# Kernel optimization log

Measured on AMD Instinct MI355X. Metric: run time of the kernel, lower is better.

The kernel has to match this reference:

```python
import jax, jax.numpy as jnp
import numpy as np
from jax import lax

B, L, C = 8, 2048, 512
H = 8
D = C // H  # head_dim = 64
FF = 4 * C


def layer_norm(x, g, b, eps=1e-5):
    mu = jnp.mean(x, axis=-1, keepdims=True)
    var = jnp.mean((x - mu) ** 2, axis=-1, keepdims=True)
    return (x - mu) * lax.rsqrt(var + eps) * g + b


def conv1d(x, w, b, groups=1):
    # x: [N, Cin, L], w: [Cout, Cin//groups, K], 'same' padding for K=3
    y = lax.conv_general_dilated(
        x, w, window_strides=(1,), padding=[(1, 1)],
        dimension_numbers=('NCH', 'OIH', 'NCH'), feature_group_count=groups)
    return y + b[None, :, None]


def setup_inputs() -> dict:
    key = jax.random.key(0)
    ks = jax.random.split(key, 12)
    s = 0.02
    inp = {
        'x': jax.random.normal(ks[0], (B, L, C), dtype=jnp.float32),
        # norm1
        'g1': jnp.ones((C,), jnp.float32), 'b1': jnp.zeros((C,), jnp.float32),
        # attention projections (stored as [in, out] for x @ W)
        'qk_w': jax.random.normal(ks[1], (C, 2 * C), jnp.float32) * s,
        'qk_b': jnp.zeros((2 * C,), jnp.float32),
        'v_w': jax.random.normal(ks[2], (C, C), jnp.float32) * s,
        'v_b': jnp.zeros((C,), jnp.float32),
        # depthwise LePE conv: [D, 1, 3], groups=D
        'lepe_w': jax.random.normal(ks[3], (D, 1, 3), jnp.float32) * s,
        'lepe_b': jnp.zeros((D,), jnp.float32),
        # norm2
        'g2': jnp.ones((C,), jnp.float32), 'b2': jnp.zeros((C,), jnp.float32),
        # GatedConv1D: inner LayerNorm + Conv1d(C, 2C, 3, pad=1); proj_out=Identity (expansion=1)
        'spn_g': jnp.ones((C,), jnp.float32), 'spn_b': jnp.zeros((C,), jnp.float32),
        'sp_cw': jax.random.normal(ks[4], (2 * C, C, 3), jnp.float32) * s,
        'sp_cb': jnp.zeros((2 * C,), jnp.float32),
        # norm3
        'g3': jnp.ones((C,), jnp.float32), 'b3': jnp.zeros((C,), jnp.float32),
        # FFN
        'w1': jax.random.normal(ks[5], (C, FF), jnp.float32) * s,
        'bb1': jnp.zeros((FF,), jnp.float32),
        'w2': jax.random.normal(ks[6], (FF, C), jnp.float32) * s,
        'bb2': jnp.zeros((C,), jnp.float32),
    }
    return inp


def _attn(x, qk_w, qk_b, v_w, v_b, lepe_w, lepe_b):
    # x: [B, L, C]
    qk = (x @ qk_w + qk_b).reshape(B, L, 2, H, D).transpose(2, 0, 3, 1, 4)
    q, k = qk[0], qk[1]                      # [B, H, L, D]
    v = (x @ v_w + v_b).reshape(B, L, H, D).transpose(0, 2, 1, 3)  # [B, H, L, D]
    q = jax.nn.elu(q) + 1.0
    k = jax.nn.elu(k) + 1.0

    def lepe(t):
        # Faithful to torch: raw row-major reshape [B,H,L,D] -> [B*H, D, L]
        # (NOT a transpose), depthwise conv along last axis, reshape back.
        c = conv1d(t.reshape(B * H, D, L), lepe_w, lepe_b, groups=D)
        return t + c.reshape(B, H, D, L).transpose(0, 1, 3, 2)

    q = lepe(q)
    k = lepe(k)
    k_mean = jnp.mean(k, axis=2, keepdims=True)                    # [B, H, 1, D]
    z = 1.0 / (jnp.einsum('bhld,bhmd->bhlm', q, k_mean) + 1e-6)    # [B, H, L, 1]
    kv = jnp.einsum('bhld,bhle->bhde', k, v) / L                   # [B, H, D, D]
    out = jnp.einsum('bhld,bhde->bhle', q, kv) * z                 # [B, H, L, D]
    return out.transpose(0, 2, 1, 3).reshape(B, L, C)


def reference(x, g1, b1, qk_w, qk_b, v_w, v_b, lepe_w, lepe_b,
              g2, b2, spn_g, spn_b, sp_cw, sp_cb, g3, b3, w1, bb1, w2, bb2):
    # Dropout is identity (eval mode).
    # Block 1: linear attention with LePE
    x = x + _attn(layer_norm(x, g1, b1), qk_w, qk_b, v_w, v_b, lepe_w, lepe_b)

    # Block 2: gated conv state path. state_path(input) = input + gated(conv(LN(input)))
    sp_in = layer_norm(x, g2, b2)
    h = layer_norm(sp_in, spn_g, spn_b)
    c = conv1d(h.transpose(0, 2, 1), sp_cw, sp_cb).transpose(0, 2, 1)  # [B, L, 2C]
    vv, gg = jnp.split(c, 2, axis=-1)
    x = x + (sp_in + vv * jax.nn.sigmoid(gg))

    # Block 3: FFN with exact GELU (torch default)
    h = layer_norm(x, g3, b3)
    x = x + (jax.nn.gelu(h @ w1 + bb1, approximate=False) @ w2 + bb2)
    return x
```

## Files before the change

### kernel.cpp

```cpp
#include <hip/hip_runtime.h>
#include <hip/hip_bf16.h>
#include <math.h>

#define Bb 8
#define Ll 2048
#define Ccn 512
#define Hh 8
#define Dd 64
#define NR (Bb * Ll)
#define PROW 2050

typedef __hip_bfloat16 bf16;
typedef __attribute__((ext_vector_type(8))) __bf16 bf16x8;
typedef __attribute__((ext_vector_type(4))) float f32x4;

#define GLDS(g, l) __builtin_amdgcn_global_load_lds(                          \
    (const __attribute__((address_space(1))) void*)(g),                       \
    (__attribute__((address_space(3))) void*)(l), 16, 0, 0)

__device__ __forceinline__ void unpack2(unsigned u, float& a, float& b) {
  union { float f; unsigned x; } lo, hi;
  lo.x = u << 16; hi.x = u & 0xffff0000u;
  a = lo.f; b = hi.f;
}

__device__ __forceinline__ float frcp(float x) { return __builtin_amdgcn_rcpf(x); }

__device__ __forceinline__ float ldin(const void* p, int i, int isbf) {
  return isbf ? (float)((const bf16*)p)[i] : ((const float*)p)[i];
}

__device__ __forceinline__ void ldin8(const void* p, size_t base, int isbf, float* v) {
  if (isbf) {
    int4 q = *(const int4*)((const bf16*)p + base);
    unpack2((unsigned)q.x, v[0], v[1]); unpack2((unsigned)q.y, v[2], v[3]);
    unpack2((unsigned)q.z, v[4], v[5]); unpack2((unsigned)q.w, v[6], v[7]);
  } else {
    float4 a = *(const float4*)((const float*)p + base);
    float4 b = *(const float4*)((const float*)p + base + 4);
    v[0]=a.x; v[1]=a.y; v[2]=a.z; v[3]=a.w;
    v[4]=b.x; v[5]=b.y; v[6]=b.z; v[7]=b.w;
  }
}

__device__ __forceinline__ void st8(bf16* dst, const float* v) {
  bf16x8 o;
#pragma unroll
  for (int t = 0; t < 8; ++t) o[t] = (__bf16)v[t];
  *(bf16x8*)dst = o;
}

__global__ void detect_kernel(const unsigned* __restrict__ g1, int* __restrict__ flag) {
  *flag = ((g1[0] & 0xFFFFu) == 0x3F80u) ? 1 : 0;
}

__global__ void ln1_kernel(const void* __restrict__ x, const void* __restrict__ g,
                           const void* __restrict__ b, const int* __restrict__ dflag,
                           bf16* __restrict__ outb, float* __restrict__ xf)
{
  int isbf = *dflag;
  int row  = blockIdx.x * 4 + (threadIdx.x >> 6);
  int lane = threadIdx.x & 63;
  size_t obase = (size_t)row * Ccn + lane * 8;
  float vals[8];
  ldin8(x, obase, isbf, vals);
  float4 c0 = {vals[0], vals[1], vals[2], vals[3]};
  float4 c1 = {vals[4], vals[5], vals[6], vals[7]};
  *(float4*)(xf + obase)     = c0;
  *(float4*)(xf + obase + 4) = c1;
  float s = 0.f, q = 0.f;
#pragma unroll
  for (int a = 0; a < 8; ++a) { s += vals[a]; q += vals[a] * vals[a]; }
#pragma unroll
  for (int off = 1; off < 64; off <<= 1) {
    s += __shfl_xor(s, off);
    q += __shfl_xor(q, off);
  }
  float mu  = s * (1.f / Ccn);
  float var = q * (1.f / Ccn) - mu * mu;
  float rs  = rsqrtf(var + 1e-5f);
  float gv[8], bv[8], o[8];
  ldin8(g, lane * 8, isbf, gv);
  ldin8(b, lane * 8, isbf, bv);
#pragma unroll
  for (int a = 0; a < 8; ++a) o[a] = (vals[a] - mu) * rs * gv[a] + bv[a];
  st8(&outb[obase], o);
}

__global__ void ln_kernel(const float* __restrict__ xin, const void* __restrict__ g,
                          const void* __restrict__ b, const int* __restrict__ dflag,
                          bf16* __restrict__ outb)
{
  int isbf = *dflag;
  int row  = blockIdx.x * 4 + (threadIdx.x >> 6);
  int lane = threadIdx.x & 63;
  const float* xr = xin + (size_t)row * Ccn;
  float4 v0 = *(const float4*)(xr + lane * 8);
  float4 v1 = *(const float4*)(xr + lane * 8 + 4);
  float vals[8] = {v0.x, v0.y, v0.z, v0.w, v1.x, v1.y, v1.z, v1.w};
  float s = 0.f, q = 0.f;
#pragma unroll
  for (int a = 0; a < 8; ++a) { s += vals[a]; q += vals[a] * vals[a]; }
#pragma unroll
  for (int off = 1; off < 64; off <<= 1) {
    s += __shfl_xor(s, off);
    q += __shfl_xor(q, off);
  }
  float mu  = s * (1.f / Ccn);
  float var = q * (1.f / Ccn) - mu * mu;
  float rs  = rsqrtf(var + 1e-5f);
  size_t obase = (size_t)row * Ccn + lane * 8;
  float gv[8], bv[8], o[8];
  ldin8(g, lane * 8, isbf, gv);
  ldin8(b, lane * 8, isbf, bv);
#pragma unroll
  for (int a = 0; a < 8; ++a) o[a] = (vals[a] - mu) * rs * gv[a] + bv[a];
  st8(&outb[obase], o);
}

__global__ void glng_kernel(float* __restrict__ xf, const bf16* __restrict__ spin,
                            const bf16* __restrict__ c, const void* __restrict__ g,
                            const void* __restrict__ b, const int* __restrict__ dflag,
                            bf16* __restrict__ outb)
{
  int isbf = *dflag;
  int row  = blockIdx.x * 4 + (threadIdx.x >> 6);
  int lane = threadIdx.x & 63;
  size_t obase = (size_t)row * Ccn + lane * 8;
  int cc = lane * 8;
  float vv[8], gg[8], sp[8], xv[8];
  ldin8(&c[(size_t)row * 1024 + cc], 0, 1, vv);
  ldin8(&c[(size_t)row * 1024 + 512 + cc], 0, 1, gg);
  ldin8(&spin[obase], 0, 1, sp);
  float4 a0 = *(const float4*)&xf[obase];
  float4 a1 = *(const float4*)&xf[obase + 4];
  xv[0]=a0.x; xv[1]=a0.y; xv[2]=a0.z; xv[3]=a0.w;
  xv[4]=a1.x; xv[5]=a1.y; xv[6]=a1.z; xv[7]=a1.w;
#pragma unroll
  for (int a = 0; a < 8; ++a) xv[a] += sp[a] + vv[a] * frcp(1.f + __expf(-gg[a]));
  float4 o0 = {xv[0], xv[1], xv[2], xv[3]};
  float4 o1 = {xv[4], xv[5], xv[6], xv[7]};
  *(float4*)&xf[obase]     = o0;
  *(float4*)&xf[obase + 4] = o1;
  float s = 0.f, q = 0.f;
#pragma unroll
  for (int a = 0; a < 8; ++a) { s += xv[a]; q += xv[a] * xv[a]; }
#pragma unroll
  for (int off = 1; off < 64; off <<= 1) {
    s += __shfl_xor(s, off);
    q += __shfl_xor(q, off);
  }
  float mu  = s * (1.f / Ccn);
  float var = q * (1.f / Ccn) - mu * mu;
  float rs  = rsqrtf(var + 1e-5f);
  float gv[8], bv[8], o[8];
  ldin8(g, lane * 8, isbf, gv);
  ldin8(b, lane * 8, isbf, bv);
#pragma unroll
  for (int a = 0; a < 8; ++a) o[a] = (xv[a] - mu) * rs * gv[a] + bv[a];
  st8(&outb[obase], o);
}

__global__ void ln2_kernel(const float* __restrict__ xin, const void* __restrict__ g,
                           const void* __restrict__ b, const void* __restrict__ sg,
                           const void* __restrict__ sb, const int* __restrict__ dflag,
                           bf16* __restrict__ sp_out, bf16* __restrict__ h_out)
{
  int isbf = *dflag;
  int row  = blockIdx.x * 4 + (threadIdx.x >> 6);
  int lane = threadIdx.x & 63;
  const float* xr = xin + (size_t)row * Ccn;
  float4 v0 = *(const float4*)(xr + lane * 8);
  float4 v1 = *(const float4*)(xr + lane * 8 + 4);
  float vals[8] = {v0.x, v0.y, v0.z, v0.w, v1.x, v1.y, v1.z, v1.w};
  float s = 0.f, q = 0.f;
#pragma unroll
  for (int a = 0; a < 8; ++a) { s += vals[a]; q += vals[a] * vals[a]; }
#pragma unroll
  for (int off = 1; off < 64; off <<= 1) {
    s += __shfl_xor(s, off);
    q += __shfl_xor(q, off);
  }
  float mu  = s * (1.f / Ccn);
  float var = q * (1.f / Ccn) - mu * mu;
  float rs  = rsqrtf(var + 1e-5f);
  size_t obase = (size_t)row * Ccn + lane * 8;
  float gv[8], bv[8], o[8];
  ldin8(g, lane * 8, isbf, gv);
  ldin8(b, lane * 8, isbf, bv);
  float s2 = 0.f, q2 = 0.f;
#pragma unroll
  for (int a = 0; a < 8; ++a) {
    o[a] = (vals[a] - mu) * rs * gv[a] + bv[a];
    s2 += o[a]; q2 += o[a] * o[a];
  }
  st8(&sp_out[obase], o);
#pragma unroll
  for (int off = 1; off < 64; off <<= 1) {
    s2 += __shfl_xor(s2, off);
    q2 += __shfl_xor(q2, off);
  }
  float mu2  = s2 * (1.f / Ccn);
  float var2 = q2 * (1.f / Ccn) - mu2 * mu2;
  float rs2  = rsqrtf(var2 + 1e-5f);
  float sgv[8], sbv[8], o2[8];
  ldin8(sg, lane * 8, isbf, sgv);
  ldin8(sb, lane * 8, isbf, sbv);
#pragma unroll
  for (int a = 0; a < 8; ++a) o2[a] = (o[a] - mu2) * rs2 * sgv[a] + sbv[a];
  size_t prow = (size_t)(row >> 11) * PROW + 1 + (row & 2047);
  st8(&h_out[prow * Ccn + lane * 8], o2);
}

__global__ void guard_zero(bf16* __restrict__ P) {
  int b = blockIdx.x;
  int t = threadIdx.x;
  size_t r0 = (size_t)b * PROW * Ccn;
  size_t r1 = r0 + (size_t)(PROW - 1) * Ccn;
  ((int*)(P + r0))[t] = 0;
  ((int*)(P + r1))[t] = 0;
}

__global__ void transpose_w(const void* __restrict__ src, bf16* __restrict__ dst,
                            const int* __restrict__ dflag, int R, int C) {
  int isbf = *dflag;
  __shared__ bf16 tile[32][33];
  int c0 = blockIdx.x * 32, r0 = blockIdx.y * 32;
  int tx = threadIdx.x & 31, ty = threadIdx.x >> 5;
#pragma unroll
  for (int i = 0; i < 32; i += 8)
    tile[ty + i][tx] = (bf16)ldin(src, (r0 + ty + i) * C + c0 + tx, isbf);
  __syncthreads();
#pragma unroll
  for (int i = 0; i < 32; i += 8)
    dst[(size_t)(c0 + ty + i) * R + r0 + tx] = tile[tx][ty + i];
}

__global__ void convw_permute(const void* __restrict__ src, bf16* __restrict__ dst,
                              const int* __restrict__ dflag) {
  int isbf = *dflag;
  int idx = blockIdx.x * 256 + threadIdx.x;
  int o = idx / 1536, j = idx - o * 1536;
  int k = j >> 9, i = j & 511;
  dst[idx] = (bf16)ldin(src, o * 1536 + i * 3 + k, isbf);
}

#define EPI_NONE  0
#define EPI_ELU1  1
#define EPI_GELU  2
#define EPI_RESID 3
#define EPI_QKV   4

template<int EPI, bool CONV>
__global__ void gemm_bt(const bf16* __restrict__ A, const bf16* __restrict__ Bt,
                        const void* __restrict__ bias, const void* __restrict__ bias2,
                        const float* __restrict__ resid,
                        void* __restrict__ out, void* __restrict__ out2,
                        const int* __restrict__ dflag,
                        int M, int Nn, int K, int orow0)
{
  int isbf = *dflag;
  __shared__ __align__(16) bf16 As[128 * 64];
  __shared__ __align__(16) bf16 Bs[128 * 64];
  int tid  = threadIdx.x;
  int wave = tid >> 6, lane = tid & 63;
  int wm = (wave >> 1) * 64, wn = (wave & 1) * 64;
  int row0 = blockIdx.x * 128;
  int col0 = blockIdx.y * 128;
  f32x4 acc[4][4] = {};
  int m_in = lane & 15;
  int kq   = lane >> 4;
  int r8   = lane >> 3;
  int swz8 = (((lane & 7) - r8) & 7) * 8;
  size_t prow0 = 0;
  if (CONV) {
    int bb = row0 >> 11, l0 = row0 & 2047;
    prow0 = (size_t)bb * PROW + l0;
  }

  for (int k0 = 0; k0 < K; k0 += 64) {
    {
      int cw = col0 + wave * 32;
#pragma unroll
      for (int g = 0; g < 4; ++g)
        GLDS(&Bt[(size_t)(cw + g*8 + r8) * K + k0 + swz8], &Bs[(wave*32 + g*8) * 64]);
    }
    if (CONV) {
      int kpos = k0 >> 9;
      int ii   = (k0 & 511) + swz8;
#pragma unroll
      for (int g = 0; g < 4; ++g) {
        size_t rs = prow0 + wave*32 + g*8 + r8 + kpos;
        GLDS(&A[rs * 512 + ii], &As[(wave*32 + g*8) * 64]);
      }
    } else {
#pragma unroll
      for (int g = 0; g < 4; ++g)
        GLDS(&A[(size_t)(row0 + wave*32 + g*8 + r8) * K + k0 + swz8],
             &As[(wave*32 + g*8) * 64]);
    }
    __syncthreads();
#pragma unroll
    for (int kk = 0; kk < 2; ++kk) {
      int Cu = kk * 4 + kq;
      bf16x8 af[4], bfr[4];
#pragma unroll
      for (int i = 0; i < 4; ++i) {
        int R = wm + i * 16 + m_in;
        af[i] = *(const bf16x8*)&As[R * 64 + ((Cu + R) & 7) * 8];
      }
#pragma unroll
      for (int j = 0; j < 4; ++j) {
        int R = wn + j * 16 + m_in;
        bfr[j] = *(const bf16x8*)&Bs[R * 64 + ((Cu + R) & 7) * 8];
      }
#pragma unroll
      for (int i = 0; i < 4; ++i)
#pragma unroll
        for (int j = 0; j < 4; ++j)
          acc[i][j] = __builtin_amdgcn_mfma_f32_16x16x32_bf16(af[i], bfr[j], acc[i][j], 0, 0, 0);
    }
    __syncthreads();
  }

  const int ESTR = 72;
  bf16* eb = As + wave * (16 * ESTR);
  int col_in = lane & 15;
  int row_in = (lane >> 4) * 4;
  int rr = lane >> 3;
  int cb = (lane & 7) * 8;
  float bvj[4];
  bool  eluj[4];
#pragma unroll
  for (int j = 0; j < 4; ++j) {
    int col = col0 + wn + j * 16 + col_in;
    if (EPI == EPI_QKV) {
      eluj[j] = (col < 1024);
      bvj[j] = eluj[j] ? ldin(bias, col, isbf) : ldin(bias2, col - 1024, isbf);
    } else {
      bvj[j] = ldin(bias, col, isbf);
      eluj[j] = false;
    }
  }
#pragma unroll
  for (int i = 0; i < 4; ++i) {
#pragma unroll
    for (int j = 0; j < 4; ++j) {
#pragma unroll
      for (int r = 0; r < 4; ++r) {
        float v = acc[i][j][r] + bvj[j];
        if (EPI == EPI_ELU1) v = (v > 0.f) ? (v + 1.f) : __expf(v);
        if (EPI == EPI_QKV && eluj[j]) v = (v > 0.f) ? (v + 1.f) : __expf(v);
        if (EPI == EPI_GELU) {
          float u = v * (0.7978845608f + 0.0356774081f * v * v);
          u = fminf(fmaxf(u, -10.f), 10.f);
          float e = __expf(2.f * u);
          v = v * e * frcp(e + 1.f);
        }
        eb[(row_in + r) * ESTR + j * 16 + col_in] = (bf16)v;
      }
    }
    int row = row0 + wm + i * 16;
#pragma unroll
    for (int s = 0; s < 2; ++s) {
      int r2 = rr + s * 8;
      bf16x8 pk = *(const bf16x8*)&eb[r2 * ESTR + cb];
      int grow = row + r2;
      int col  = col0 + wn + cb;
      if (EPI == EPI_RESID) {
        size_t gbase = (size_t)(grow + orow0) * Nn + col;
        float4 ra = *(const float4*)&resid[gbase];
        float4 rb = *(const float4*)&resid[gbase + 4];
        float vv[8];
#pragma unroll
        for (int t = 0; t < 8; ++t) vv[t] = (float)pk[t];
        vv[0]+=ra.x; vv[1]+=ra.y; vv[2]+=ra.z; vv[3]+=ra.w;
        vv[4]+=rb.x; vv[5]+=rb.y; vv[6]+=rb.z; vv[7]+=rb.w;
        if (isbf) {
          st8(&((bf16*)out)[gbase], vv);
        } else {
          float4 o0 = {vv[0], vv[1], vv[2], vv[3]};
          float4 o1 = {vv[4], vv[5], vv[6], vv[7]};
          *(float4*)&((float*)out)[gbase]     = o0;
          *(float4*)&((float*)out)[gbase + 4] = o1;
        }
      } else if (EPI == EPI_QKV) {
        if (col < 1024)
          *(bf16x8*)&((bf16*)out)[(size_t)grow * 1024 + col] = pk;
        else
          *(bf16x8*)&((bf16*)out2)[(size_t)grow * 512 + (col - 1024)] = pk;
      } else {
        *(bf16x8*)&((bf16*)out)[(size_t)grow * Nn + col] = pk;
      }
    }
  }
}

template<int SRCOFF, int DSTSTR, bool DOKM>
__global__ void lepe2_kernel(const bf16* __restrict__ qk, bf16* __restrict__ dst,
                             const void* __restrict__ w, const void* __restrict__ cb,
                             const int* __restrict__ dflag, float* __restrict__ km) {
  int isbf = *dflag;
  __shared__ float buf[64][66];
  int bh = blockIdx.y; int b = bh >> 3, h = bh & 7;
  int tile = blockIdx.x;
  int t = threadIdx.x;
  int r  = t >> 3;
  int o8 = (t & 7) * 8;
  size_t sbase = (size_t)b * 2048 * 1024 + SRCOFF + h * 64;

  int4 cv[2], id[2];
#pragma unroll
  for (int it = 0; it < 2; ++it) {
    int ch = r + it * 32;
    cv[it] = *(const int4*)&qk[sbase + (size_t)(ch * 32 + tile) * 1024 + o8];
    id[it] = *(const int4*)&qk[sbase + (size_t)(tile * 64 + ch) * 1024 + o8];
  }
  float edge = 0.f; int eidx = -1, espot = 0;
  if (t < 64) {
    eidx = t; espot = 0;
    if (tile > 0) edge = (float)qk[sbase + (size_t)(t * 32 + tile - 1) * 1024 + 63];
  } else if (t < 128) {
    eidx = t - 64; espot = 65;
    if (tile < 31) edge = (float)qk[sbase + (size_t)((t - 64) * 32 + tile + 1) * 1024 + 0];
  }
  float w0[2], w1[2], w2[2], bi[2];
#pragma unroll
  for (int it = 0; it < 2; ++it) {
    int ch = r + it * 32;
    w0[it] = ldin(w, ch * 3 + 0, isbf);
    w1[it] = ldin(w, ch * 3 + 1, isbf);
    w2[it] = ldin(w, ch * 3 + 2, isbf);
    bi[it] = ldin(cb, ch, isbf);
  }
#pragma unroll
  for (int it = 0; it < 2; ++it) {
    float v[8];
    unpack2((unsigned)cv[it].x, v[0], v[1]); unpack2((unsigned)cv[it].y, v[2], v[3]);
    unpack2((unsigned)cv[it].z, v[4], v[5]); unpack2((unsigned)cv[it].w, v[6], v[7]);
    int ch = r + it * 32;
#pragma unroll
    for (int k = 0; k < 8; ++k) buf[ch][1 + o8 + k] = v[k];
  }
  if (eidx >= 0) buf[eidx][espot] = edge;
  __syncthreads();
  float co[2][8];
#pragma unroll
  for (int it = 0; it < 2; ++it) {
    int ch = r + it * 32;
    float a0 = buf[ch][o8], a1 = buf[ch][o8 + 1];
#pragma unroll
    for (int k = 0; k < 8; ++k) {
      float a2 = buf[ch][o8 + 2 + k];
      co[it][k] = bi[it] + w0[it] * a0 + w1[it] * a1 + w2[it] * a2;
      a0 = a1; a1 = a2;
    }
  }
  __syncthreads();
#pragma unroll
  for (int it = 0; it < 2; ++it) {
    int ch = r + it * 32;
#pragma unroll
    for (int k = 0; k < 8; ++k) buf[o8 + k][ch] = co[it][k];
  }
  __syncthreads();
  float psum[8];
#pragma unroll
  for (int k = 0; k < 8; ++k) psum[k] = 0.f;
#pragma unroll
  for (int it = 0; it < 2; ++it) {
    int lr = r + it * 32;
    float v[8];
    unpack2((unsigned)id[it].x, v[0], v[1]); unpack2((unsigned)id[it].y, v[2], v[3]);
    unpack2((unsigned)id[it].z, v[4], v[5]); unpack2((unsigned)id[it].w, v[6], v[7]);
#pragma unroll
    for (int k = 0; k < 8; ++k) {
      v[k] += buf[lr][o8 + k];
      if (DOKM) psum[k] += v[k];
    }
    st8(&dst[(size_t)(b * 2048 + tile * 64 + lr) * DSTSTR + h * 64 + o8], v);
  }
  if (DOKM) {
    __syncthreads();
#pragma unroll
    for (int k = 0; k < 8; ++k) buf[r][o8 + k] = psum[k];
    __syncthreads();
    if (t < 64) {
      float s = 0.f;
#pragma unroll 8
      for (int rr2 = 0; rr2 < 32; ++rr2) s += buf[rr2][t];
      atomicAdd(&km[bh * 64 + t], s * (1.f / 2048.f));
    }
  }
}

__global__ void kv_kernel(const bf16* __restrict__ k2, const bf16* __restrict__ v,
                          float* __restrict__ kv) {
  int bh = blockIdx.x, split = blockIdx.y;
  int b = bh >> 3, h = bh & 7;
  int t = threadIdx.x;
  __shared__ __align__(16) bf16 ks[64][64];
  __shared__ __align__(16) bf16 vs[64][64];
  int d0 = (t & 15) * 4, e0 = (t >> 4) * 4;
  int lr = t >> 2, q4 = (t & 3) * 16;
  float acc[4][4] = {};
  for (int chunk = 0; chunk < 4; ++chunk) {
    int l = split * 256 + chunk * 64 + lr;
    size_t rk = ((size_t)(b*2048 + l)) * 1024 + h*64 + q4;
    size_t rv = ((size_t)(b*2048 + l)) * 512 + h*64 + q4;
    *(int4*)&ks[lr][q4]     = *(const int4*)&k2[rk];
    *(int4*)&ks[lr][q4 + 8] = *(const int4*)&k2[rk + 8];
    *(int4*)&vs[lr][q4]     = *(const int4*)&v[rv];
    *(int4*)&vs[lr][q4 + 8] = *(const int4*)&v[rv + 8];
    __syncthreads();
    for (int l2 = 0; l2 < 64; ++l2) {
      float kvv[4], vvv[4];
      int2 kp = *(const int2*)&ks[l2][d0];
      int2 vp = *(const int2*)&vs[l2][e0];
      unpack2((unsigned)kp.x, kvv[0], kvv[1]); unpack2((unsigned)kp.y, kvv[2], kvv[3]);
      unpack2((unsigned)vp.x, vvv[0], vvv[1]); unpack2((unsigned)vp.y, vvv[2], vvv[3]);
#pragma unroll
      for (int a = 0; a < 4; ++a)
#pragma unroll
        for (int c = 0; c < 4; ++c) acc[a][c] += kvv[a] * vvv[c];
    }
    __syncthreads();
  }
  const float sc = 1.f / 2048.f;
#pragma unroll
  for (int a = 0; a < 4; ++a)
#pragma unroll
    for (int c = 0; c < 4; ++c)
      atomicAdd(&kv[(size_t)(bh*64 + d0 + a) * 64 + e0 + c], acc[a][c] * sc);
}

__global__ void attn_out_kernel(const bf16* __restrict__ q2, const float* __restrict__ kv,
                                const float* __restrict__ kmean, float* __restrict__ xf) {
  int bh = blockIdx.x; int b = bh >> 3, h = bh & 7;
  int lbase = blockIdx.y * 64;
  int t = threadIdx.x;
  __shared__ float kvs[64][68];
  __shared__ float km[64];
  for (int i = t; i < 64*64; i += 256) kvs[i >> 6][i & 63] = kv[(size_t)bh*4096 + i];
  if (t < 64) km[t] = kmean[bh*64 + t];
  __syncthreads();
  int lr = t >> 2, eg = (t & 3) * 16;
  int l = lbase + lr;
  size_t qrow = ((size_t)(b*2048 + l)) * 512 + h*64;
  float qv[64];
#pragma unroll
  for (int d8 = 0; d8 < 64; d8 += 8) {
    int4 p = *(const int4*)&q2[qrow + d8];
    unpack2((unsigned)p.x, qv[d8+0], qv[d8+1]);
    unpack2((unsigned)p.y, qv[d8+2], qv[d8+3]);
    unpack2((unsigned)p.z, qv[d8+4], qv[d8+5]);
    unpack2((unsigned)p.w, qv[d8+6], qv[d8+7]);
  }
  float zd = 0.f;
#pragma unroll
  for (int d = 0; d < 64; ++d) zd += qv[d] * km[d];
  float z = frcp(zd + 1e-6f);
  float sacc[16] = {};
#pragma unroll
  for (int d = 0; d < 64; ++d) {
    float qd = qv[d];
    const float4* row = (const float4*)&kvs[d][eg];
    float4 r0 = row[0], r1 = row[1], r2 = row[2], r3 = row[3];
    sacc[0]  += qd * r0.x; sacc[1]  += qd * r0.y; sacc[2]  += qd * r0.z; sacc[3]  += qd * r0.w;
    sacc[4]  += qd * r1.x; sacc[5]  += qd * r1.y; sacc[6]  += qd * r1.z; sacc[7]  += qd * r1.w;
    sacc[8]  += qd * r2.x; sacc[9]  += qd * r2.y; sacc[10] += qd * r2.z; sacc[11] += qd * r2.w;
    sacc[12] += qd * r3.x; sacc[13] += qd * r3.y; sacc[14] += qd * r3.z; sacc[15] += qd * r3.w;
  }
  size_t xrow = ((size_t)(b*2048 + l)) * 512 + h*64 + eg;
#pragma unroll
  for (int s = 0; s < 4; ++s) {
    float4 cur = *(const float4*)&xf[xrow + s * 4];
    cur.x += sacc[s*4+0] * z; cur.y += sacc[s*4+1] * z;
    cur.z += sacc[s*4+2] * z; cur.w += sacc[s*4+3] * z;
    *(float4*)&xf[xrow + s * 4] = cur;
  }
}

__global__ void gating_kernel(float* __restrict__ xf, const bf16* __restrict__ spin,
                              const bf16* __restrict__ c) {
  size_t idx = ((size_t)blockIdx.x * 256 + threadIdx.x) * 8;
  size_t n = idx >> 9; int cc = (int)(idx & 511);
  float vv[8], gg[8], sp[8];
  ldin8(&c[n * 1024 + cc], 0, 1, vv);
  ldin8(&c[n * 1024 + 512 + cc], 0, 1, gg);
  ldin8(&spin[idx], 0, 1, sp);
#pragma unroll
  for (int s = 0; s < 2; ++s) {
    float4 cur = *(const float4*)&xf[idx + s * 4];
    float* cp = &cur.x;
#pragma unroll
    for (int t = 0; t < 4; ++t) {
      int a = s * 4 + t;
      cp[t] += sp[a] + vv[a] * frcp(1.f + __expf(-gg[a]));
    }
    *(float4*)&xf[idx + s * 4] = cur;
  }
}

extern "C" void kernel_launch(void* const* d_in, const int* in_sizes, int n_in,
                              void* d_out, int out_size, void* d_ws, size_t ws_size,
                              hipStream_t stream) {
  (void)in_sizes; (void)n_in; (void)out_size;
  const void* x      = d_in[0];
  const void* g1     = d_in[1];
  const void* b1     = d_in[2];
  const void* qk_w   = d_in[3];
  const void* qk_b   = d_in[4];
  const void* v_w    = d_in[5];
  const void* v_b    = d_in[6];
  const void* lepe_w = d_in[7];
  const void* lepe_b = d_in[8];
  const void* g2     = d_in[9];
  const void* b2     = d_in[10];
  const void* spn_g  = d_in[11];
  const void* spn_b  = d_in[12];
  const void* sp_cw  = d_in[13];
  const void* sp_cb  = d_in[14];
  const void* g3     = d_in[15];
  const void* b3     = d_in[16];
  const void* w1     = d_in[17];
  const void* bb1    = d_in[18];
  const void* w2     = d_in[19];
  const void* bb2    = d_in[20];

  char* ws = (char*)d_ws;
  const size_t MB = 1 << 20;
  const bool big = ws_size >= (size_t)129 * MB;

  bf16*  qk_wT  = (bf16*)(ws);
  bf16*  v_wT   = (bf16*)(ws + 0x100000);
  bf16*  convWT = (bf16*)(ws + 0x180000);
  bf16*  w1T    = (bf16*)(ws + 0x480000);
  bf16*  w2T    = (bf16*)(ws + 0x680000);
  float* kmean  = (float*)(ws + 0x880000);
  float* kvb    = (float*)(ws + 0x890000);
  int*   dflag  = (int*)(ws + 0x990000);
  float* xf     = (float*)(ws + 16*MB);
  bf16*  ybf    = (bf16*)(ws + 48*MB);
  bf16*  qkbuf  = (bf16*)(ws + 64*MB);
  bf16*  spbuf  = ybf;
  bf16*  ybf2p  = (bf16*)(ws + 64*MB);
  bf16*  cbufS  = (bf16*)(ws + 96*MB);
  bf16*  cbufB  = (bf16*)(ws + 96*MB);
  bf16*  tbuf   = (bf16*)(ws + 64*MB);
  bf16*  vout   = (bf16*)d_out;

  detect_kernel<<<1, 1, 0, stream>>>((const unsigned*)g1, dflag);
  hipMemsetAsync(kvb, 0, 64 * 64 * 64 * sizeof(float), stream);
  hipMemsetAsync(kmean, 0, 64 * 64 * sizeof(float), stream);

  transpose_w<<<dim3(32, 16), 256, 0, stream>>>(qk_w, qk_wT, dflag, 512, 1024);
  transpose_w<<<dim3(16, 16), 256, 0, stream>>>(v_w,  v_wT,  dflag, 512, 512);
  transpose_w<<<dim3(64, 16), 256, 0, stream>>>(w1,   w1T,   dflag, 512, 2048);
  transpose_w<<<dim3(16, 64), 256, 0, stream>>>(w2,   w2T,   dflag, 2048, 512);
  convw_permute<<<1024*1536/256, 256, 0, stream>>>(sp_cw, convWT, dflag);

  ln1_kernel<<<NR/4, 256, 0, stream>>>(x, g1, b1, dflag, ybf, xf);
  gemm_bt<EPI_QKV, false><<<dim3(128, 12), 256, 0, stream>>>(
      ybf, qk_wT, qk_b, v_b, nullptr, qkbuf, vout, dflag, NR, 1536, 512, 0);
  lepe2_kernel<0,   512,  false><<<dim3(32, 64), 256, 0, stream>>>(
      qkbuf, ybf, lepe_w, lepe_b, dflag, nullptr);
  lepe2_kernel<512, 1024, true ><<<dim3(32, 64), 256, 0, stream>>>(
      qkbuf, qkbuf, lepe_w, lepe_b, dflag, kmean);
  kv_kernel<<<dim3(64, 8), 256, 0, stream>>>(qkbuf, vout, kvb);
  attn_out_kernel<<<dim3(64, 32), 256, 0, stream>>>(ybf, kvb, kmean, xf);

  guard_zero<<<8, 256, 0, stream>>>(ybf2p);
  ln2_kernel<<<NR/4, 256, 0, stream>>>(xf, g2, b2, spn_g, spn_b, dflag, spbuf, ybf2p);
  if (big) {
    gemm_bt<EPI_NONE, true><<<dim3(128, 8), 256, 0, stream>>>(
        ybf2p, convWT, sp_cb, nullptr, nullptr, cbufB, nullptr, dflag, NR, 1024, 1536, 0);
    glng_kernel<<<NR/4, 256, 0, stream>>>(xf, spbuf, cbufB, g3, b3, dflag, ybf);
  } else {
    for (int half = 0; half < 2; ++half) {
      size_t ro = (size_t)half * 8192;
      gemm_bt<EPI_NONE, true><<<dim3(64, 8), 256, 0, stream>>>(
          ybf2p + (ro >> 11) * PROW * 512, convWT, sp_cb, nullptr, nullptr,
          cbufS, nullptr, dflag, 8192, 1024, 1536, 0);
      gating_kernel<<<8192*512/2048, 256, 0, stream>>>(xf + ro*512, spbuf + ro*512, cbufS);
    }
    ln_kernel<<<NR/4, 256, 0, stream>>>(xf, g3, b3, dflag, ybf);
  }

  if (big) {
    gemm_bt<EPI_GELU,  false><<<dim3(128, 16), 256, 0, stream>>>(
        ybf, w1T, bb1, nullptr, nullptr, tbuf, nullptr, dflag, NR, 2048, 512, 0);
    gemm_bt<EPI_RESID, false><<<dim3(128, 4),  256, 0, stream>>>(
        tbuf, w2T, bb2, nullptr, xf, d_out, nullptr, dflag, NR, 512, 2048, 0);
  } else {
    for (int half = 0; half < 2; ++half) {
      size_t ro = (size_t)half * 8192;
      gemm_bt<EPI_GELU,  false><<<dim3(64, 16), 256, 0, stream>>>(
          ybf + ro*512, w1T, bb1, nullptr, nullptr, tbuf, nullptr, dflag, 8192, 2048, 512, 0);
      gemm_bt<EPI_RESID, false><<<dim3(64, 4),  256, 0, stream>>>(
          tbuf, w2T, bb2, nullptr, xf, d_out, nullptr, dflag, 8192, 512, 2048, (int)ro);
    }
  }
}
```

Baseline: 460.2 us.

## Add 256x256-tile 8-wave pipelined GEMM for QKV, conv and FFN1

Adds a new GEMM kernel with 256x256 output tiles, 512 threads and 128 KB of LDS. It double-buffers tiles through direct global-to-LDS loads with XOR-style swizzling, and spreads each stage's loads across four phases that overlap with MFMA compute. The kernel replaces the 128x128 gemm_bt for the QKV projection, the conv-as-GEMM and the first FFN GEMM, while the residual GEMM stays on the old kernel. Larger tiles cut global traffic per FLOP and raise data reuse. In exchange, grids shrink (as few as 128 blocks in the small path), occupancy is limited to one block per CU, and so wave-level parallelism may be too low to fill the 256 CUs.

```diff
diff --git a/kernel.cpp b/kernel.cpp
--- a/kernel.cpp
+++ b/kernel.cpp
@@ -250,6 +250,177 @@
 #define EPI_GELU  2
 #define EPI_RESID 3
 #define EPI_QKV   4
+
+template<int EPI, bool CONV>
+__global__ __launch_bounds__(512)
+void gemm8(const bf16* __restrict__ A, const bf16* __restrict__ Bt,
+           const void* __restrict__ bias, const void* __restrict__ bias2,
+           void* __restrict__ out, void* __restrict__ out2,
+           const int* __restrict__ dflag, int Nn, int K)
+{
+  __shared__ __align__(16) bf16 lds[65536];
+  int tid  = threadIdx.x;
+  int wave = tid >> 6, lane = tid & 63;
+  int wr = wave >> 2, wc = wave & 3;
+  int row0 = blockIdx.x * 256;
+  int col0 = blockIdx.y * 256;
+  f32x4 acc[8][4] = {};
+  int m_in = lane & 15;
+  int kq   = lane >> 4;
+  int r8   = lane >> 3;
+  int swz8 = (((lane & 7) - r8) & 7) * 8;
+  int NT = K >> 6;
+  size_t prow0 = 0;
+  if (CONV) prow0 = (size_t)(row0 >> 11) * PROW + (row0 & 2047);
+
+#define AOFS(buf) ((buf) * 32768)
+#define BOFS(buf) ((buf) * 32768 + 16384)
+#define STG_A(buf, half, T) do { if ((T) < NT) {                               \
+    int lr0 = (half) * 128 + wave * 16;                                        \
+    if (CONV) {                                                                \
+      int kpos = ((T) << 6) >> 9, ii = (((T) << 6) & 511) + swz8;              \
+      GLDS(&A[(prow0 + lr0 + r8 + kpos) * 512 + ii],                           \
+           &lds[AOFS(buf) + (lr0) * 64]);                                      \
+      GLDS(&A[(prow0 + lr0 + 8 + r8 + kpos) * 512 + ii],                       \
+           &lds[AOFS(buf) + (lr0 + 8) * 64]);                                  \
+    } else {                                                                   \
+      GLDS(&A[(size_t)(row0 + lr0 + r8) * K + ((T) << 6) + swz8],              \
+           &lds[AOFS(buf) + (lr0) * 64]);                                      \
+      GLDS(&A[(size_t)(row0 + lr0 + 8 + r8) * K + ((T) << 6) + swz8],          \
+           &lds[AOFS(buf) + (lr0 + 8) * 64]);                                  \
+    } } } while (0)
+#define STG_B(buf, half, T) do { if ((T) < NT) {                               \
+    int lr0 = (half) * 128 + wave * 16;                                        \
+    GLDS(&Bt[(size_t)(col0 + lr0 + r8) * K + ((T) << 6) + swz8],               \
+         &lds[BOFS(buf) + (lr0) * 64]);                                        \
+    GLDS(&Bt[(size_t)(col0 + lr0 + 8 + r8) * K + ((T) << 6) + swz8],           \
+         &lds[BOFS(buf) + (lr0 + 8) * 64]);                                    \
+    } } while (0)
+
+  bf16x8 bfr[4][2];
+#define LDB8(buf) do {                                                         \
+    _Pragma("unroll") for (int n = 0; n < 4; ++n) {                            \
+      int R = wc * 64 + n * 16 + m_in;                                         \
+      _Pragma("unroll") for (int kk = 0; kk < 2; ++kk)                         \
+        bfr[n][kk] = *(const bf16x8*)&lds[BOFS(buf) + R * 64 +                 \
+                                          (((kk * 4 + kq) + R) & 7) * 8];      \
+    } } while (0)
+
+#define PHASE(q, buf, STAGECODE, DOW, FULL) do {                               \
+    bf16x8 af[2][2];                                                           \
+    _Pragma("unroll") for (int mi = 0; mi < 2; ++mi) {                         \
+      int R = wr * 128 + (q) * 32 + mi * 16 + m_in;                            \
+      _Pragma("unroll") for (int kk = 0; kk < 2; ++kk)                         \
+        af[mi][kk] = *(const bf16x8*)&lds[AOFS(buf) + R * 64 +                 \
+                                          (((kk * 4 + kq) + R) & 7) * 8];      \
+    }                                                                          \
+    if ((q) == 0) LDB8(buf);                                                   \
+    STAGECODE;                                                                 \
+    asm volatile("" ::: "memory");                                             \
+    __builtin_amdgcn_s_barrier();                                              \
+    asm volatile("" ::: "memory");                                             \
+    __builtin_amdgcn_s_setprio(1);                                             \
+    _Pragma("unroll") for (int mi = 0; mi < 2; ++mi)                           \
+      _Pragma("unroll") for (int n = 0; n < 4; ++n)                            \
+        _Pragma("unroll") for (int kk = 0; kk < 2; ++kk)                       \
+          acc[2 * (q) + mi][n] = __builtin_amdgcn_mfma_f32_16x16x32_bf16(      \
+              af[mi][kk], bfr[n][kk], acc[2 * (q) + mi][n], 0, 0, 0);          \
+    __builtin_amdgcn_s_setprio(0);                                             \
+    if (DOW) {                                                                 \
+      if (FULL) asm volatile("s_waitcnt vmcnt(4)" ::: "memory");               \
+      else      asm volatile("s_waitcnt vmcnt(0)" ::: "memory");               \
+    }                                                                          \
+    asm volatile("" ::: "memory");                                             \
+    __builtin_amdgcn_s_barrier();                                              \
+    asm volatile("" ::: "memory");                                             \
+  } while (0)
+
+  STG_B(0, 0, 0); STG_B(0, 1, 0);
+  STG_A(0, 0, 0); STG_A(0, 1, 0);
+  STG_B(1, 0, 1); STG_B(1, 1, 1);
+  asm volatile("s_waitcnt vmcnt(4)" ::: "memory");
+  __builtin_amdgcn_s_barrier();
+  asm volatile("" ::: "memory");
+
+  int NI = NT >> 1;
+  for (int it = 0; it < NI; ++it) {
+    int Ta = 2 * it + 1, Tb = 2 * it + 2, Tc = 2 * it + 3;
+    bool f4 = (Tb < NT);
+    bool f8 = (Tc < NT);
+    PHASE(0, 0, { STG_A(1, 0, Ta); }, 0, true);
+    PHASE(1, 0, { STG_A(1, 1, Ta); }, 0, true);
+    PHASE(2, 0, { STG_B(0, 0, Tb); }, 0, true);
+    PHASE(3, 0, { STG_B(0, 1, Tb); }, 1, f4);
+    PHASE(0, 1, { STG_A(0, 0, Tb); }, 0, true);
+    PHASE(1, 1, { STG_A(0, 1, Tb); }, 0, true);
+    PHASE(2, 1, { STG_B(1, 0, Tc); }, 0, true);
+    PHASE(3, 1, { STG_B(1, 1, Tc); }, 1, f8);
+  }
+  asm volatile("s_waitcnt vmcnt(0)" ::: "memory");
+  __syncthreads();
+#undef PHASE
+#undef LDB8
+#undef STG_A
+#undef STG_B
+#undef AOFS
+#undef BOFS
+
+  int isbf = *dflag;
+  const int ESTR = 72;
+  bf16* eb = lds + wave * (16 * ESTR);
+  int col_in = lane & 15;
+  int row_in = (lane >> 4) * 4;
+  int rr = lane >> 3;
+  int cb = (lane & 7) * 8;
+  int wm = wr * 128, wn = wc * 64;
+  float bvj[4];
+  bool  eluj[4];
+#pragma unroll
+  for (int j = 0; j < 4; ++j) {
+    int col = col0 + wn + j * 16 + col_in;
+    if (EPI == EPI_QKV) {
+      eluj[j] = (col < 1024);
+      bvj[j] = eluj[j] ? ldin(bias, col, isbf) : ldin(bias2, col - 1024, isbf);
+    } else {
+      bvj[j] = ldin(bias, col, isbf);
+      eluj[j] = false;
+    }
+  }
+#pragma unroll
+  for (int i = 0; i < 8; ++i) {
+#pragma unroll
+    for (int j = 0; j < 4; ++j) {
+#pragma unroll
+      for (int r = 0; r < 4; ++r) {
+        float v = acc[i][j][r] + bvj[j];
+        if (EPI == EPI_QKV && eluj[j]) v = (v > 0.f) ? (v + 1.f) : __expf(v);
+        if (EPI == EPI_GELU) {
+          float u = v * (0.7978845608f + 0.0356774081f * v * v);
+          u = fminf(fmaxf(u, -10.f), 10.f);
+          float e = __expf(2.f * u);
+          v = v * e * frcp(e + 1.f);
+        }
+        eb[(row_in + r) * ESTR + j * 16 + col_in] = (bf16)v;
+      }
+    }
+    int row = row0 + wm + i * 16;
+#pragma unroll
+    for (int s = 0; s < 2; ++s) {
+      int r2 = rr + s * 8;
+      bf16x8 pk = *(const bf16x8*)&eb[r2 * ESTR + cb];
+      int grow = row + r2;
+      int col  = col0 + wn + cb;
+      if (EPI == EPI_QKV) {
+        if (col < 1024)
+          *(bf16x8*)&((bf16*)out)[(size_t)grow * 1024 + col] = pk;
+        else
+          *(bf16x8*)&((bf16*)out2)[(size_t)grow * 512 + (col - 1024)] = pk;
+      } else {
+        *(bf16x8*)&((bf16*)out)[(size_t)grow * Nn + col] = pk;
+      }
+    }
+  }
+}
 
 template<int EPI, bool CONV>
 __global__ void gemm_bt(const bf16* __restrict__ A, const bf16* __restrict__ Bt,
@@ -661,8 +832,8 @@
   convw_permute<<<1024*1536/256, 256, 0, stream>>>(sp_cw, convWT, dflag);
 
   ln1_kernel<<<NR/4, 256, 0, stream>>>(x, g1, b1, dflag, ybf, xf);
-  gemm_bt<EPI_QKV, false><<<dim3(128, 12), 256, 0, stream>>>(
-      ybf, qk_wT, qk_b, v_b, nullptr, qkbuf, vout, dflag, NR, 1536, 512, 0);
+  gemm8<EPI_QKV, false><<<dim3(64, 6), 512, 0, stream>>>(
+      ybf, qk_wT, qk_b, v_b, qkbuf, vout, dflag, 1536, 512);
   lepe2_kernel<0,   512,  false><<<dim3(32, 64), 256, 0, stream>>>(
       qkbuf, ybf, lepe_w, lepe_b, dflag, nullptr);
   lepe2_kernel<512, 1024, true ><<<dim3(32, 64), 256, 0, stream>>>(
@@ -673,30 +844,30 @@
   guard_zero<<<8, 256, 0, stream>>>(ybf2p);
   ln2_kernel<<<NR/4, 256, 0, stream>>>(xf, g2, b2, spn_g, spn_b, dflag, spbuf, ybf2p);
   if (big) {
-    gemm_bt<EPI_NONE, true><<<dim3(128, 8), 256, 0, stream>>>(
-        ybf2p, convWT, sp_cb, nullptr, nullptr, cbufB, nullptr, dflag, NR, 1024, 1536, 0);
+    gemm8<EPI_NONE, true><<<dim3(64, 4), 512, 0, stream>>>(
+        ybf2p, convWT, sp_cb, nullptr, cbufB, nullptr, dflag, 1024, 1536);
     glng_kernel<<<NR/4, 256, 0, stream>>>(xf, spbuf, cbufB, g3, b3, dflag, ybf);
   } else {
     for (int half = 0; half < 2; ++half) {
       size_t ro = (size_t)half * 8192;
-      gemm_bt<EPI_NONE, true><<<dim3(64, 8), 256, 0, stream>>>(
-          ybf2p + (ro >> 11) * PROW * 512, convWT, sp_cb, nullptr, nullptr,
-          cbufS, nullptr, dflag, 8192, 1024, 1536, 0);
+      gemm8<EPI_NONE, true><<<dim3(32, 4), 512, 0, stream>>>(
+          ybf2p + (ro >> 11) * PROW * 512, convWT, sp_cb, nullptr,
+          cbufS, nullptr, dflag, 1024, 1536);
       gating_kernel<<<8192*512/2048, 256, 0, stream>>>(xf + ro*512, spbuf + ro*512, cbufS);
     }
     ln_kernel<<<NR/4, 256, 0, stream>>>(xf, g3, b3, dflag, ybf);
   }
 
   if (big) {
-    gemm_bt<EPI_GELU,  false><<<dim3(128, 16), 256, 0, stream>>>(
-        ybf, w1T, bb1, nullptr, nullptr, tbuf, nullptr, dflag, NR, 2048, 512, 0);
+    gemm8<EPI_GELU, false><<<dim3(64, 8), 512, 0, stream>>>(
+        ybf, w1T, bb1, nullptr, tbuf, nullptr, dflag, 2048, 512);
     gemm_bt<EPI_RESID, false><<<dim3(128, 4),  256, 0, stream>>>(
         tbuf, w2T, bb2, nullptr, xf, d_out, nullptr, dflag, NR, 512, 2048, 0);
   } else {
     for (int half = 0; half < 2; ++half) {
       size_t ro = (size_t)half * 8192;
-      gemm_bt<EPI_GELU,  false><<<dim3(64, 16), 256, 0, stream>>>(
-          ybf + ro*512, w1T, bb1, nullptr, nullptr, tbuf, nullptr, dflag, 8192, 2048, 512, 0);
+      gemm8<EPI_GELU, false><<<dim3(32, 8), 512, 0, stream>>>(
+          ybf + ro*512, w1T, bb1, nullptr, tbuf, nullptr, dflag, 2048, 512);
       gemm_bt<EPI_RESID, false><<<dim3(64, 4),  256, 0, stream>>>(
           tbuf, w2T, bb2, nullptr, xf, d_out, nullptr, dflag, 8192, 512, 2048, (int)ro);
     }
```

Result: slower. 474.2 us (+3.0%).
